# Kernel optimization log

Hardware: AMD Instinct MI355X
Metric: run time of the kernel (lower is better)

Reference implementation:

```python
import jax, jax.numpy as jnp
import numpy as np
import math

# Static problem sizes (match input_specs)
B, TQ, SQ, TK, SK = 1, 8, 256, 32, 1024
DM, NH = 1024, 8
HD = DM // NH            # 128; mrope_section sums to HD//2
MROPE = [16, 24, 24]
ROPE_BASE = 10000.0


def _build_indices():
    """Reproduce create_idx_cube + slow/fast index selection (all static)."""
    T_max = max(TQ, TK)
    H_max = int(math.sqrt(max(SQ, SK)))
    cube = np.stack(np.meshgrid(np.arange(T_max), np.arange(H_max), np.arange(H_max), indexing='ij'), axis=-1)  # (T,H,W,3)
    # slow (query) indices
    t_idx = np.linspace(0, T_max - 1, TQ).astype(int)
    slow = cube[t_idx]
    if SQ < SK:
        h_q = int(math.sqrt(SQ))
        hi = np.linspace(0, H_max, 2 * h_q + 1).astype(int)[1:-1][::2]
        slow = slow[:, hi][:, :, hi]
    # fast (key) indices
    h_k = int(math.sqrt(SK))
    hf = np.linspace(0, H_max, 2 * h_k + 1).astype(int)[1:-1][::2]
    fast = cube[:, hf][:, :, hf]
    return slow.reshape(-1, 3).T, fast.reshape(-1, 3).T, max(T_max, H_max)


_slow_np, _fast_np, _SEQ = _build_indices()
SLOW_POS = jnp.asarray(_slow_np)   # (3, TQ*SQ) int
FAST_POS = jnp.asarray(_fast_np)   # (3, TK*SK) int

# Standard rotary tables: cos/sin of shape (seq_len, HD)
_inv = 1.0 / (ROPE_BASE ** (np.arange(0, HD, 2, dtype=np.float32) / HD))
_freqs = np.outer(np.arange(_SEQ, dtype=np.float32), _inv)
_emb = np.concatenate([_freqs, _freqs], axis=-1)
COS = jnp.asarray(np.cos(_emb), dtype=jnp.float32)
SIN = jnp.asarray(np.sin(_emb), dtype=jnp.float32)

# per-channel axis (t/h/w) selector, equivalent to the split/concat with i%3
AXIS_MAP = jnp.asarray(np.concatenate([np.full(m, i % 3) for i, m in enumerate(MROPE * 2)]))  # (HD,)


def rotate_half(x):
    return jnp.concatenate([-x[..., HD // 2:], x[..., :HD // 2]], axis=-1)


def apply_mrope(x, pos):
    # x: (B, NH, N, HD); pos: (3, N)
    cos_g = jnp.take_along_axis(COS[pos], AXIS_MAP[None, None, :], axis=0)[0]  # (N, HD)
    sin_g = jnp.take_along_axis(SIN[pos], AXIS_MAP[None, None, :], axis=0)[0]
    return x * cos_g[None, None] + rotate_half(x) * sin_g[None, None]


def setup_inputs() -> dict:
    key = jax.random.key(0)
    ks = jax.random.split(key, 9)
    s = 0.02
    return {
        'q': jax.random.normal(ks[0], (B, TQ, SQ, DM), jnp.float32),
        'k': jax.random.normal(ks[1], (B, TK, SK, DM), jnp.float32),
        'v': jax.random.normal(ks[2], (B, TK, SK, DM), jnp.float32),
        'Wq': jax.random.normal(ks[3], (DM, DM), jnp.float32) * s,
        'bq': jnp.zeros((DM,), jnp.float32),
        'Wk': jax.random.normal(ks[4], (DM, DM), jnp.float32) * s,
        'bk': jnp.zeros((DM,), jnp.float32),
        'Wv': jax.random.normal(ks[5], (DM, DM), jnp.float32) * s,
        'bv': jnp.zeros((DM,), jnp.float32),
    }


def reference(q, k, v, Wq, bq, Wk, bk, Wv, bv):
    # QKV projections -> (B, NH, N, HD)
    qh = (q.reshape(B, TQ * SQ, DM) @ Wq + bq).reshape(B, TQ * SQ, NH, HD).transpose(0, 2, 1, 3)
    kh = (k.reshape(B, TK * SK, DM) @ Wk + bk).reshape(B, TK * SK, NH, HD).transpose(0, 2, 1, 3)
    vh = (v.reshape(B, TK * SK, DM) @ Wv + bv).reshape(B, TK * SK, NH, HD).transpose(0, 2, 1, 3)
    # multimodal 3D RoPE on q (slow frames) and k (fast frames)
    qh = apply_mrope(qh, SLOW_POS)
    kh = apply_mrope(kh, FAST_POS)
    # group time: each query frame attends to its r = TK//TQ aligned kv frames
    r = TK // TQ
    qg = qh.reshape(NH, TQ, SQ, HD).transpose(1, 0, 2, 3)          # (TQ, NH, SQ, HD)
    kg = kh.reshape(NH, TQ, r * SK, HD).transpose(1, 0, 2, 3)      # (TQ, NH, r*SK, HD)
    vg = vh.reshape(NH, TQ, r * SK, HD).transpose(1, 0, 2, 3)
    scores = jnp.einsum('thqd,thkd->thqk', qg, kg) / math.sqrt(HD)
    attn = jax.nn.softmax(scores, axis=-1)
    out = jnp.einsum('thqk,thkd->thqd', attn, vg)                  # (TQ, NH, SQ, HD)
    return out.transpose(0, 2, 1, 3).reshape(B, TQ, SQ, DM)
```

## Files before the change

### kernel.cpp

```cpp
#include <hip/hip_runtime.h>

typedef __bf16 bf16;
typedef __bf16 bf16x8 __attribute__((ext_vector_type(8)));
typedef float  f32x4  __attribute__((ext_vector_type(4)));

#define MFMA16(a, b, c) __builtin_amdgcn_mfma_f32_16x16x32_bf16((a), (b), (c), 0, 0, 0)

#define GLOAD_LDS16(gptr, lptr)                                              \
    __builtin_amdgcn_global_load_lds(                                        \
        (const __attribute__((address_space(1))) unsigned int*)(gptr),       \
        (__attribute__((address_space(3))) unsigned int*)(lptr), 16, 0, 0)

constexpr int kDM = 1024;
constexpr int kNTOK = 32768;

static __device__ inline f32x4 zero4() { f32x4 z = {0.f, 0.f, 0.f, 0.f}; return z; }

__global__ __launch_bounds__(256) void cvt_qk(
    const float* __restrict__ q, const float* __restrict__ k, bf16* __restrict__ dst)
{
    const int q8 = 262144, tot = q8 + 4194304;
    int idx = blockIdx.x * 256 + threadIdx.x;
    const int stride = gridDim.x * 256;
    for (; idx < tot; idx += stride) {
        const float* s = (idx < q8) ? q + (size_t)idx * 8
                                    : k + (size_t)(idx - q8) * 8;
        const float4 u0 = *(const float4*)s;
        const float4 u1 = *(const float4*)(s + 4);
        bf16x8 w;
        w[0] = (bf16)u0.x; w[1] = (bf16)u0.y; w[2] = (bf16)u0.z; w[3] = (bf16)u0.w;
        w[4] = (bf16)u1.x; w[5] = (bf16)u1.y; w[6] = (bf16)u1.z; w[7] = (bf16)u1.w;
        *(bf16x8*)&dst[(size_t)idx * 8] = w;
    }
}

__global__ __launch_bounds__(256) void cvt_bf16(
    const float* __restrict__ src, bf16* __restrict__ dst, int n8)
{
    int idx = blockIdx.x * 256 + threadIdx.x;
    const int stride = gridDim.x * 256;
    for (; idx < n8; idx += stride) {
        const float4 u0 = *(const float4*)(src + (size_t)idx * 8);
        const float4 u1 = *(const float4*)(src + (size_t)idx * 8 + 4);
        bf16x8 w;
        w[0] = (bf16)u0.x; w[1] = (bf16)u0.y; w[2] = (bf16)u0.z; w[3] = (bf16)u0.w;
        w[4] = (bf16)u1.x; w[5] = (bf16)u1.y; w[6] = (bf16)u1.z; w[7] = (bf16)u1.w;
        *(bf16x8*)&dst[(size_t)idx * 8] = w;
    }
}

__global__ __launch_bounds__(256) void transpose_all(
    const float* __restrict__ Wq, const float* __restrict__ Wk,
    const float* __restrict__ Wv, bf16* __restrict__ Wqt,
    bf16* __restrict__ Wkt, bf16* __restrict__ Wvt)
{
    __shared__ bf16 T[64][68];
    const float* W = (blockIdx.z == 0) ? Wq : (blockIdx.z == 1) ? Wk : Wv;
    bf16* Wt       = (blockIdx.z == 0) ? Wqt : (blockIdx.z == 1) ? Wkt : Wvt;
    const int tid = threadIdx.x;
    const int n0 = blockIdx.x * 64, k0 = blockIdx.y * 64;
    #pragma unroll
    for (int i = 0; i < 4; i++) {
        const int kk = (tid >> 4) + i * 16, nn4 = (tid & 15) * 4;
        float4 v = *(const float4*)&W[(size_t)(k0 + kk) * kDM + n0 + nn4];
        T[nn4 + 0][kk] = (bf16)v.x; T[nn4 + 1][kk] = (bf16)v.y;
        T[nn4 + 2][kk] = (bf16)v.z; T[nn4 + 3][kk] = (bf16)v.w;
    }
    __syncthreads();
    #pragma unroll
    for (int i = 0; i < 4; i++) {
        const int nn = (tid >> 4) + i * 16, kc = (tid & 15) * 4;
        *(ushort4*)&Wt[(size_t)(n0 + nn) * kDM + k0 + kc] = *(const ushort4*)&T[nn][kc];
    }
}

template <int MODE>
__global__ __launch_bounds__(256) void gemm_fused(
    const bf16* __restrict__ Xb, const bf16* __restrict__ Wt,
    const float* __restrict__ bias, bf16* __restrict__ out, int mtiles_per_xcd)
{
    __shared__ char smem[65536];
    bf16* Y = (bf16*)smem;

    const int b    = blockIdx.x;
    const int xcd  = b & 7;
    const int s    = b >> 3;
    const int m0   = (xcd * mtiles_per_xcd + (s >> 3)) * 128;
    const int n0   = (s & 7) * 128;
    const int tid  = threadIdx.x;
    const int wave = tid >> 6;
    const int lane = tid & 63;
    const int quad = lane >> 4, l16 = lane & 15;
    const int mb   = (wave & 1) * 64, nb = (wave >> 1) * 64;
    const int r8   = lane >> 3, j8 = lane & 7;

    f32x4 acc[4][4];
    #pragma unroll
    for (int i = 0; i < 4; i++)
        #pragma unroll
        for (int j = 0; j < 4; j++) acc[i][j] = zero4();

    auto stage = [&](int k0, char* buf) {
        bf16* Ab = (bf16*)buf;
        bf16* Bb = (bf16*)(buf + 16384);
        #pragma unroll
        for (int i = 0; i < 4; i++) {
            const int c = wave * 4 + i;
            const int row = c * 8 + r8;
            const int off = (j8 ^ (row & 7)) * 8;
            GLOAD_LDS16(&Xb[(size_t)(m0 + row) * kDM + k0 + off], &Ab[c * 512]);
            GLOAD_LDS16(&Wt[(size_t)(n0 + row) * kDM + k0 + off], &Bb[c * 512]);
        }
    };

    stage(0, smem);
    asm volatile("s_waitcnt vmcnt(0)" ::: "memory");
    __builtin_amdgcn_s_barrier();

    for (int t = 0; t < 16; ++t) {
        const char* cur = smem + (t & 1) * 32768;
        if (t < 15) stage((t + 1) * 64, smem + ((t + 1) & 1) * 32768);
        __builtin_amdgcn_sched_barrier(0);

        const bf16* Ab = (const bf16*)cur;
        const bf16* Bb = (const bf16*)(cur + 16384);
        #pragma unroll
        for (int ks = 0; ks < 2; ks++) {
            const int G = ks * 4 + quad;
            bf16x8 a[4], bfr[4];
            #pragma unroll
            for (int i = 0; i < 4; i++)
                a[i] = *(const bf16x8*)&Ab[(mb + i * 16 + l16) * 64 + ((G ^ (l16 & 7)) * 8)];
            #pragma unroll
            for (int j = 0; j < 4; j++)
                bfr[j] = *(const bf16x8*)&Bb[(nb + j * 16 + l16) * 64 + ((G ^ (l16 & 7)) * 8)];
            #pragma unroll
            for (int i = 0; i < 4; i++)
                #pragma unroll
                for (int j = 0; j < 4; j++)
                    acc[i][j] = MFMA16(a[i], bfr[j], acc[i][j]);
        }

        if (t < 15) asm volatile("s_waitcnt vmcnt(0)" ::: "memory");
        __builtin_amdgcn_sched_barrier(0);
        __builtin_amdgcn_s_barrier();
    }

    __syncthreads();

    if (MODE == 3) {
        #pragma unroll
        for (int j = 0; j < 4; j++) {
            const int n = nb + j * 16 + l16;
            const float bv = bias[n0 + n];
            #pragma unroll
            for (int i = 0; i < 4; i++) {
                const int m = mb + i * 16 + quad * 4;
                bf16 tmp[4];
                #pragma unroll
                for (int r = 0; r < 4; r++) tmp[r] = (bf16)(acc[i][j][r] + bv);
                *(ushort4*)&Y[n * 136 + m] = *(const ushort4*)tmp;
            }
        }
        __syncthreads();
        const int row = tid >> 1, seg = (tid & 1) * 64;
        #pragma unroll
        for (int kk = 0; kk < 8; kk++)
            *(uint4*)&out[(size_t)(n0 + row) * kNTOK + m0 + seg + kk * 8] =
                *(const uint4*)&Y[row * 136 + seg + kk * 8];
    } else {
        if (wave >= 2) {
            #pragma unroll
            for (int j = 0; j < 4; j++) {
                const int dcol = 64 + j * 16 + l16;
                const float bv = bias[n0 + dcol];
                #pragma unroll
                for (int i = 0; i < 4; i++)
                    #pragma unroll
                    for (int r = 0; r < 4; r++)
                        Y[(mb + i * 16 + quad * 4 + r) * 136 + dcol] =
                            (bf16)(acc[i][j][r] + bv);
            }
        }
        __syncthreads();
        if (wave < 2) {
            #pragma unroll
            for (int j = 0; j < 4; j++) {
                const int d = j * 16 + l16;
                const float bv = bias[n0 + d];
                const float invf = exp2f((float)d * -0.20762050593045951f);
                #pragma unroll
                for (int i = 0; i < 4; i++) {
                    #pragma unroll
                    for (int r = 0; r < 4; r++) {
                        const int mloc = mb + i * 16 + quad * 4 + r;
                        const int tok = m0 + mloc;
                        int pt, ph, pw;
                        if (MODE == 2) { pt = tok >> 10; ph = (tok >> 5) & 31; pw = tok & 31; }
                        else { int tq = tok >> 8; pt = (31 * tq) / 7;
                               ph = 2 * ((tok >> 4) & 15) + 1; pw = 2 * (tok & 15) + 1; }
                        const int p = (d < 16) ? pt : ((d < 40) ? ph : pw);
                        float sn, cs;
                        __sincosf((float)p * invf, &sn, &cs);
                        const float x1 = acc[i][j][r] + bv;
                        const float x2 = (float)Y[mloc * 136 + 64 + d];
                        Y[mloc * 136 + d]      = (bf16)(x1 * cs - x2 * sn);
                        Y[mloc * 136 + 64 + d] = (bf16)(x2 * cs + x1 * sn);
                    }
                }
            }
        }
        __syncthreads();
        const int row = tid >> 1, seg = (tid & 1) * 64;
        #pragma unroll
        for (int kk = 0; kk < 8; kk++)
            *(uint4*)&out[(size_t)(m0 + row) * kDM + n0 + seg + kk * 8] =
                *(const uint4*)&Y[row * 136 + seg + kk * 8];
    }
}

__global__ __launch_bounds__(256) void attn_kernel(
    const bf16* __restrict__ qh, const bf16* __restrict__ kh,
    const bf16* __restrict__ vt, float* __restrict__ Opart, float* __restrict__ ml)
{
    __shared__ bf16 Ks[64 * 128];
    __shared__ bf16 Vs[128 * 64];
    __shared__ bf16 Ps[4][16][64];

    const int tid  = threadIdx.x;
    const int b    = blockIdx.x;
    const int j    = b >> 3;
    const int g    = (b & 7) * 32 + (j >> 2);
    const int qb   = j & 3;
    const int h    = g & 7;
    const int z    = g >> 3;
    const int t    = z >> 2, sp = z & 3;
    const int wave = tid >> 6;
    const int lane = tid & 63;
    const int quad = lane >> 4, l16 = lane & 15;

    const int qrow = qb * 64 + wave * 16 + l16;
    const size_t qbase = ((size_t)(t * 256 + qrow)) * kDM + h * 128;
    bf16x8 aq[4];
    #pragma unroll
    for (int kb = 0; kb < 4; kb++)
        aq[kb] = *(const bf16x8*)&qh[qbase + kb * 32 + quad * 8];

    bf16x8 ones;
    #pragma unroll
    for (int e = 0; e < 8; e++) ones[e] = (bf16)1.0f;

    f32x4 o[9];
    #pragma unroll
    for (int j2 = 0; j2 < 9; j2++) o[j2] = zero4();
    float m_run[4];
    #pragma unroll
    for (int r = 0; r < 4; r++) m_run[r] = -1e30f;
    const float scale = 0.08838834764831845f;

    const int r16 = lane >> 4, j16 = lane & 15;
    const int r8  = lane >> 3, j8  = lane & 7;

    for (int kt = 0; kt < 16; kt++) {
        const int kbase = t * 4096 + sp * 1024 + kt * 64;
        __syncthreads();
        #pragma unroll
        for (int i = 0; i < 4; i++) {
            const int c = wave * 4 + i;
            const int krow = c * 4 + r16;
            GLOAD_LDS16(&kh[(size_t)(kbase + krow) * kDM + h * 128 + ((j16 ^ (krow & 15)) * 8)],
                        &Ks[c * 512]);
        }
        #pragma unroll
        for (int i = 0; i < 4; i++) {
            const int c = wave * 4 + i;
            GLOAD_LDS16(&vt[(size_t)(h * 128 + c * 8 + r8) * kNTOK + kbase + ((j8 ^ r8) * 8)],
                        &Vs[c * 512]);
        }
        __syncthreads();

        f32x4 s[4];
        #pragma unroll
        for (int c = 0; c < 4; c++) s[c] = zero4();
        __builtin_amdgcn_s_setprio(1);
        #pragma unroll
        for (int kb = 0; kb < 4; kb++) {
            #pragma unroll
            for (int c = 0; c < 4; c++) {
                bf16x8 bfr = *(const bf16x8*)&Ks[(c * 16 + l16) * 128 + (((kb * 4 + quad) ^ l16) * 8)];
                s[c] = MFMA16(aq[kb], bfr, s[c]);
            }
        }
        __builtin_amdgcn_s_setprio(0);

        float alpha[4];
        #pragma unroll
        for (int r = 0; r < 4; r++) {
            float sv[4];
            #pragma unroll
            for (int c = 0; c < 4; c++) sv[c] = s[c][r] * scale;
            float mx = fmaxf(fmaxf(sv[0], sv[1]), fmaxf(sv[2], sv[3]));
            #pragma unroll
            for (int off = 1; off < 16; off <<= 1) mx = fmaxf(mx, __shfl_xor(mx, off));
            const float mn = fmaxf(m_run[r], mx);
            alpha[r] = __expf(m_run[r] - mn);
            m_run[r] = mn;
            const int q7 = quad * 4 + r;
            #pragma unroll
            for (int c = 0; c < 4; c++) {
                const int col = (c * 16 + l16) ^ ((q7 & 7) * 8);
                Ps[wave][q7][col] = (bf16)__expf(sv[c] - mn);
            }
        }
        #pragma unroll
        for (int j2 = 0; j2 < 9; j2++)
            #pragma unroll
            for (int r = 0; r < 4; r++) o[j2][r] *= alpha[r];
        __builtin_amdgcn_s_setprio(1);
        #pragma unroll
        for (int ks = 0; ks < 2; ks++) {
            bf16x8 pa = *(const bf16x8*)&Ps[wave][l16][((ks * 4 + quad) ^ (l16 & 7)) * 8];
            #pragma unroll
            for (int j2 = 0; j2 < 8; j2++) {
                bf16x8 bv = *(const bf16x8*)&Vs[(j2 * 16 + l16) * 64 + (((ks * 4 + quad) ^ (l16 & 7)) * 8)];
                o[j2] = MFMA16(pa, bv, o[j2]);
            }
            o[8] = MFMA16(pa, ones, o[8]);
        }
        __builtin_amdgcn_s_setprio(0);
    }

    #pragma unroll
    for (int r = 0; r < 4; r++) {
        const int srow = qb * 64 + wave * 16 + quad * 4 + r;
        const size_t pr = ((size_t)(z * 8 + h)) * 256 + srow;
        #pragma unroll
        for (int j2 = 0; j2 < 8; j2++)
            Opart[pr * 128 + j2 * 16 + l16] = o[j2][r];
        if (l16 == 0) { ml[pr * 2] = m_run[r]; ml[pr * 2 + 1] = o[8][r]; }
    }
}

__global__ __launch_bounds__(256) void combine_kernel(
    const float* __restrict__ Opart, const float* __restrict__ ml,
    float* __restrict__ out)
{
    const int tid = threadIdx.x;
    const int rid = blockIdx.x * 2 + (tid >> 7);
    const int d   = tid & 127;
    const int t = rid >> 11, h = (rid >> 8) & 7, srow = rid & 255;

    float mv[4], lv[4];
    #pragma unroll
    for (int sp = 0; sp < 4; sp++) {
        const size_t pr = ((size_t)((t * 4 + sp) * 8 + h)) * 256 + srow;
        float2 p = *(const float2*)&ml[pr * 2];
        mv[sp] = p.x; lv[sp] = p.y;
    }
    const float ms = fmaxf(fmaxf(mv[0], mv[1]), fmaxf(mv[2], mv[3]));
    float lsum = 0.f, acc = 0.f;
    #pragma unroll
    for (int sp = 0; sp < 4; sp++) {
        const size_t pr = ((size_t)((t * 4 + sp) * 8 + h)) * 256 + srow;
        const float w = __expf(mv[sp] - ms);
        lsum += lv[sp] * w;
        acc  += Opart[pr * 128 + d] * w;
    }
    out[((size_t)(t * 256 + srow)) * kDM + h * 128 + d] = acc / lsum;
}

extern "C" void kernel_launch(void* const* d_in, const int* in_sizes, int n_in,
                              void* d_out, int out_size, void* d_ws, size_t ws_size,
                              hipStream_t stream)
{
    const float* q  = (const float*)d_in[0];
    const float* k  = (const float*)d_in[1];
    const float* v  = (const float*)d_in[2];
    const float* Wq = (const float*)d_in[3];
    const float* bq = (const float*)d_in[4];
    const float* Wk = (const float*)d_in[5];
    const float* bk = (const float*)d_in[6];
    const float* Wv = (const float*)d_in[7];
    const float* bv = (const float*)d_in[8];
    float* out = (float*)d_out;

    bf16* qh  = (bf16*)d_ws;
    bf16* kh  = qh + (size_t)2048 * 1024;
    bf16* vt  = kh + (size_t)32768 * 1024;
    bf16* Wqt = vt + (size_t)32768 * 1024;
    bf16* Wkt = Wqt + (size_t)1024 * 1024;
    bf16* Wvt = Wkt + (size_t)1024 * 1024;
    float* Opart = (float*)(Wvt + (size_t)1024 * 1024);
    float* ml    = Opart + (size_t)32 * 8 * 256 * 128;
    bf16* Xb     = (bf16*)(ml + (size_t)32 * 8 * 256 * 2);
    bf16* Xq     = Xb;
    bf16* Xk     = Xb + (size_t)2048 * 1024;

    transpose_all<<<dim3(16, 16, 3), 256, 0, stream>>>(Wq, Wk, Wv, Wqt, Wkt, Wvt);

    cvt_qk<<<2048, 256, 0, stream>>>(q, k, Xb);
    gemm_fused<1><<<128,  256, 0, stream>>>(Xq, Wqt, bq, qh, 2);
    gemm_fused<2><<<2048, 256, 0, stream>>>(Xk, Wkt, bk, kh, 32);

    cvt_bf16<<<2048, 256, 0, stream>>>(v, Xb, 32768 * 1024 / 8);
    gemm_fused<3><<<2048, 256, 0, stream>>>(Xb, Wvt, bv, vt, 32);

    attn_kernel<<<1024, 256, 0, stream>>>(qh, kh, vt, Opart, ml);
    combine_kernel<<<8192, 256, 0, stream>>>(Opart, ml, out);
}
```

Measured before the change: 611.9 us.

## Merge Q/K/V conversions and projection GEMMs into single grouped launches

Combines the separate fp32-to-bf16 conversion kernels for q, k and v into one launch, and the three templated projection GEMM launches into one grouped kernel that picks its operands and epilogue mode from the block index. This removes launch gaps and the small Q GEMM's tail, and lets the V work overlap with the K work. In exchange the epilogue mode becomes a runtime branch instead of a template constant, which may raise register pressure. The workspace also needs a separate bf16 buffer for v instead of reusing the q/k buffer.

Result: slower. 645.5 us (+5.5%).

```diff
diff --git a/kernel.cpp b/kernel.cpp
--- a/kernel.cpp
+++ b/kernel.cpp
@@ -16,15 +16,19 @@
 
 static __device__ inline f32x4 zero4() { f32x4 z = {0.f, 0.f, 0.f, 0.f}; return z; }
 
-__global__ __launch_bounds__(256) void cvt_qk(
-    const float* __restrict__ q, const float* __restrict__ k, bf16* __restrict__ dst)
-{
-    const int q8 = 262144, tot = q8 + 4194304;
+__global__ __launch_bounds__(256) void cvt_all(
+    const float* __restrict__ q, const float* __restrict__ k,
+    const float* __restrict__ v, bf16* __restrict__ dst)
+{
+    const int q8 = 262144, k8 = 4194304;
+    const int tot = q8 + 2 * k8;
     int idx = blockIdx.x * 256 + threadIdx.x;
     const int stride = gridDim.x * 256;
     for (; idx < tot; idx += stride) {
-        const float* s = (idx < q8) ? q + (size_t)idx * 8
-                                    : k + (size_t)(idx - q8) * 8;
+        const float* s;
+        if (idx < q8)            s = q + (size_t)idx * 8;
+        else if (idx < q8 + k8)  s = k + (size_t)(idx - q8) * 8;
+        else                     s = v + (size_t)(idx - q8 - k8) * 8;
         const float4 u0 = *(const float4*)s;
         const float4 u1 = *(const float4*)(s + 4);
         bf16x8 w;
@@ -34,21 +38,6 @@
     }
 }
 
-__global__ __launch_bounds__(256) void cvt_bf16(
-    const float* __restrict__ src, bf16* __restrict__ dst, int n8)
-{
-    int idx = blockIdx.x * 256 + threadIdx.x;
-    const int stride = gridDim.x * 256;
-    for (; idx < n8; idx += stride) {
-        const float4 u0 = *(const float4*)(src + (size_t)idx * 8);
-        const float4 u1 = *(const float4*)(src + (size_t)idx * 8 + 4);
-        bf16x8 w;
-        w[0] = (bf16)u0.x; w[1] = (bf16)u0.y; w[2] = (bf16)u0.z; w[3] = (bf16)u0.w;
-        w[4] = (bf16)u1.x; w[5] = (bf16)u1.y; w[6] = (bf16)u1.z; w[7] = (bf16)u1.w;
-        *(bf16x8*)&dst[(size_t)idx * 8] = w;
-    }
-}
-
 __global__ __launch_bounds__(256) void transpose_all(
     const float* __restrict__ Wq, const float* __restrict__ Wk,
     const float* __restrict__ Wv, bf16* __restrict__ Wqt,
@@ -74,18 +63,27 @@
     }
 }
 
-template <int MODE>
-__global__ __launch_bounds__(256) void gemm_fused(
-    const bf16* __restrict__ Xb, const bf16* __restrict__ Wt,
-    const float* __restrict__ bias, bf16* __restrict__ out, int mtiles_per_xcd)
+__global__ __launch_bounds__(256) void gemm_all(
+    const bf16* __restrict__ Xq, const bf16* __restrict__ Xk,
+    const bf16* __restrict__ Xv, const bf16* __restrict__ Wqt,
+    const bf16* __restrict__ Wkt, const bf16* __restrict__ Wvt,
+    const float* __restrict__ bq, const float* __restrict__ bk,
+    const float* __restrict__ bv, bf16* __restrict__ qh,
+    bf16* __restrict__ kh, bf16* __restrict__ vt)
 {
     __shared__ char smem[65536];
     bf16* Y = (bf16*)smem;
 
-    const int b    = blockIdx.x;
+    int b = blockIdx.x;
+    const bf16* X; const bf16* Wt; const float* bias; bf16* out;
+    int mtiles, mode;
+    if (b < 2048)      { X = Xk; Wt = Wkt; bias = bk; out = kh; mtiles = 32; mode = 2; }
+    else if (b < 4096) { b -= 2048; X = Xv; Wt = Wvt; bias = bv; out = vt; mtiles = 32; mode = 3; }
+    else               { b -= 4096; X = Xq; Wt = Wqt; bias = bq; out = qh; mtiles = 2;  mode = 1; }
+
     const int xcd  = b & 7;
     const int s    = b >> 3;
-    const int m0   = (xcd * mtiles_per_xcd + (s >> 3)) * 128;
+    const int m0   = (xcd * mtiles + (s >> 3)) * 128;
     const int n0   = (s & 7) * 128;
     const int tid  = threadIdx.x;
     const int wave = tid >> 6;
@@ -108,7 +106,7 @@
             const int c = wave * 4 + i;
             const int row = c * 8 + r8;
             const int off = (j8 ^ (row & 7)) * 8;
-            GLOAD_LDS16(&Xb[(size_t)(m0 + row) * kDM + k0 + off], &Ab[c * 512]);
+            GLOAD_LDS16(&X[(size_t)(m0 + row) * kDM + k0 + off],  &Ab[c * 512]);
             GLOAD_LDS16(&Wt[(size_t)(n0 + row) * kDM + k0 + off], &Bb[c * 512]);
         }
     };
@@ -148,17 +146,17 @@
 
     __syncthreads();
 
-    if (MODE == 3) {
+    if (mode == 3) {
         #pragma unroll
         for (int j = 0; j < 4; j++) {
             const int n = nb + j * 16 + l16;
-            const float bv = bias[n0 + n];
+            const float bv2 = bias[n0 + n];
             #pragma unroll
             for (int i = 0; i < 4; i++) {
                 const int m = mb + i * 16 + quad * 4;
                 bf16 tmp[4];
                 #pragma unroll
-                for (int r = 0; r < 4; r++) tmp[r] = (bf16)(acc[i][j][r] + bv);
+                for (int r = 0; r < 4; r++) tmp[r] = (bf16)(acc[i][j][r] + bv2);
                 *(ushort4*)&Y[n * 136 + m] = *(const ushort4*)tmp;
             }
         }
@@ -173,13 +171,13 @@
             #pragma unroll
             for (int j = 0; j < 4; j++) {
                 const int dcol = 64 + j * 16 + l16;
-                const float bv = bias[n0 + dcol];
+                const float bv2 = bias[n0 + dcol];
                 #pragma unroll
                 for (int i = 0; i < 4; i++)
                     #pragma unroll
                     for (int r = 0; r < 4; r++)
                         Y[(mb + i * 16 + quad * 4 + r) * 136 + dcol] =
-                            (bf16)(acc[i][j][r] + bv);
+                            (bf16)(acc[i][j][r] + bv2);
             }
         }
         __syncthreads();
@@ -187,7 +185,7 @@
             #pragma unroll
             for (int j = 0; j < 4; j++) {
                 const int d = j * 16 + l16;
-                const float bv = bias[n0 + d];
+                const float bv2 = bias[n0 + d];
                 const float invf = exp2f((float)d * -0.20762050593045951f);
                 #pragma unroll
                 for (int i = 0; i < 4; i++) {
@@ -196,13 +194,13 @@
                         const int mloc = mb + i * 16 + quad * 4 + r;
                         const int tok = m0 + mloc;
                         int pt, ph, pw;
-                        if (MODE == 2) { pt = tok >> 10; ph = (tok >> 5) & 31; pw = tok & 31; }
+                        if (mode == 2) { pt = tok >> 10; ph = (tok >> 5) & 31; pw = tok & 31; }
                         else { int tq = tok >> 8; pt = (31 * tq) / 7;
                                ph = 2 * ((tok >> 4) & 15) + 1; pw = 2 * (tok & 15) + 1; }
                         const int p = (d < 16) ? pt : ((d < 40) ? ph : pw);
                         float sn, cs;
                         __sincosf((float)p * invf, &sn, &cs);
-                        const float x1 = acc[i][j][r] + bv;
+                        const float x1 = acc[i][j][r] + bv2;
                         const float x2 = (float)Y[mloc * 136 + 64 + d];
                         Y[mloc * 136 + d]      = (bf16)(x1 * cs - x2 * sn);
                         Y[mloc * 136 + 64 + d] = (bf16)(x2 * cs + x1 * sn);
@@ -322,8 +320,8 @@
             bf16x8 pa = *(const bf16x8*)&Ps[wave][l16][((ks * 4 + quad) ^ (l16 & 7)) * 8];
             #pragma unroll
             for (int j2 = 0; j2 < 8; j2++) {
-                bf16x8 bv = *(const bf16x8*)&Vs[(j2 * 16 + l16) * 64 + (((ks * 4 + quad) ^ (l16 & 7)) * 8)];
-                o[j2] = MFMA16(pa, bv, o[j2]);
+                bf16x8 bv2 = *(const bf16x8*)&Vs[(j2 * 16 + l16) * 64 + (((ks * 4 + quad) ^ (l16 & 7)) * 8)];
+                o[j2] = MFMA16(pa, bv2, o[j2]);
             }
             o[8] = MFMA16(pa, ones, o[8]);
         }
@@ -392,19 +390,14 @@
     bf16* Wvt = Wkt + (size_t)1024 * 1024;
     float* Opart = (float*)(Wvt + (size_t)1024 * 1024);
     float* ml    = Opart + (size_t)32 * 8 * 256 * 128;
-    bf16* Xb     = (bf16*)(ml + (size_t)32 * 8 * 256 * 2);
-    bf16* Xq     = Xb;
-    bf16* Xk     = Xb + (size_t)2048 * 1024;
+    bf16* Xq     = (bf16*)(ml + (size_t)32 * 8 * 256 * 2);
+    bf16* Xk     = Xq + (size_t)2048 * 1024;
+    bf16* Xv     = Xk + (size_t)32768 * 1024;
 
     transpose_all<<<dim3(16, 16, 3), 256, 0, stream>>>(Wq, Wk, Wv, Wqt, Wkt, Wvt);
-
-    cvt_qk<<<2048, 256, 0, stream>>>(q, k, Xb);
-    gemm_fused<1><<<128,  256, 0, stream>>>(Xq, Wqt, bq, qh, 2);
-    gemm_fused<2><<<2048, 256, 0, stream>>>(Xk, Wkt, bk, kh, 32);
-
-    cvt_bf16<<<2048, 256, 0, stream>>>(v, Xb, 32768 * 1024 / 8);
-    gemm_fused<3><<<2048, 256, 0, stream>>>(Xb, Wvt, bv, vt, 32);
-
+    cvt_all<<<4096, 256, 0, stream>>>(q, k, v, Xq);
+    gemm_all<<<4224, 256, 0, stream>>>(Xq, Xk, Xv, Wqt, Wkt, Wvt,
+                                       bq, bk, bv, qh, kh, vt);
     attn_kernel<<<1024, 256, 0, stream>>>(qh, kh, vt, Opart, ml);
     combine_kernel<<<8192, 256, 0, stream>>>(Opart, ml, out);
 }
```
